# Kernel tuning notes

Measured on AMD Instinct MI355X. Metric: run time of the kernel, lower is better.

Reference implementation:

```python
import jax, jax.numpy as jnp
import numpy as np

B, CIN, NH, W, L, K = 16, 64, 64, 32, 4, 5
EPS = 1e-5
FORGET_BIAS = 1.0


def conv(x, w, b=None):
    # x: [B,C,H,W], w: [O,I,k,k] -> SAME padding, stride 1 (NCHW)
    y = jax.lax.conv_general_dilated(x, w, (1, 1), 'SAME',
                                     dimension_numbers=('NCHW', 'OIHW', 'NCHW'))
    if b is not None:
        y = y + b[None, :, None, None]
    return y


def ln(x, g, b):
    # torch LayerNorm([C,W,W]): normalize each sample over (C,H,W)
    m = jnp.mean(x, axis=(1, 2, 3), keepdims=True)
    v = jnp.mean((x - m) ** 2, axis=(1, 2, 3), keepdims=True)
    return (x - m) * jax.lax.rsqrt(v + EPS) * g[None] + b[None]


def attn_channel(q, kv):
    # q: [B,C,W,H], kv: [B,L,C,W,H]
    b, c, w, h = q.shape
    qf = q.reshape(b, c, w * h)                 # [B,C,HW]
    kf = kv.reshape(b, -1, w * h)               # [B,L*C,HW]
    a = jax.nn.softmax(jnp.einsum('bcp,blp->bcl', qf, kf), axis=2)  # [B,C,L*C]
    out = jnp.einsum('bcl,blp->bcp', a, kf)     # [B,C,HW]
    return out.reshape(b, c, w, h)


def attn_spatial(q, kv):
    # q: [B,C,W,H], kv: [B,L,C,W,H]
    b, c, w, h = q.shape
    qf = q.reshape(b, c, w * h).transpose(0, 2, 1)          # [B,HW,C]
    kf = kv.transpose(0, 1, 3, 4, 2).reshape(b, -1, c)      # [B,L*HW,C]
    a = jax.nn.softmax(jnp.einsum('bpc,bqc->bpq', qf, kf), axis=2)  # [B,HW,L*HW]
    out = jnp.einsum('bpq,bqc->bpc', a, kf)                 # [B,HW,C]
    return out.reshape(b, w, h, c).transpose(0, 3, 1, 2)


def setup_inputs() -> dict:
    key = jax.random.key(0)
    ks = iter(jax.random.split(key, 64))
    rn = lambda shape, s=1.0: jax.random.normal(next(ks), shape, jnp.float32) * s
    ones = lambda shape: jnp.ones(shape, jnp.float32)
    zeros = lambda shape: jnp.zeros(shape, jnp.float32)
    s = 0.02
    d = {}
    d['x_t'] = rn((B, CIN, W, W))
    d['h_t'] = rn((B, NH, W, W))
    d['c_t'] = rn((B, NH, W, W))
    d['c_historys'] = rn((B, L, NH, W, W))
    d['m_t'] = rn((B, NH, W, W))
    d['w_x'] = rn((7 * NH, CIN, K, K), s); d['ln_x_g'] = ones((7 * NH, W, W)); d['ln_x_b'] = zeros((7 * NH, W, W))
    d['w_h'] = rn((4 * NH, NH, K, K), s);  d['ln_h_g'] = ones((4 * NH, W, W)); d['ln_h_b'] = zeros((4 * NH, W, W))
    d['w_m'] = rn((3 * NH, NH, K, K), s);  d['ln_m_g'] = ones((3 * NH, W, W)); d['ln_m_b'] = zeros((3 * NH, W, W))
    d['w_o'] = rn((NH, 2 * NH, K, K), s);  d['ln_o_g'] = ones((NH, W, W));     d['ln_o_b'] = zeros((NH, W, W))
    d['w_last'] = rn((NH, 2 * NH, 1, 1), s)
    d['s_norm_g'] = ones((NH, W, W)); d['s_norm_b'] = zeros((NH, W, W))
    d['c_norm_g'] = ones((NH, W, W)); d['c_norm_b'] = zeros((NH, W, W))
    d['ca_w1'] = rn((NH, NH, K, K), s); d['ca_b1'] = zeros((NH,))
    d['ca_ln_g'] = ones((NH, W, W));    d['ca_ln_b'] = zeros((NH, W, W))
    d['ca_w2'] = rn((NH, NH, 1, 1), s); d['ca_b2'] = zeros((NH,))
    d['sa_w1'] = rn((NH, NH, K, K), s)
    d['sa_ln_g'] = ones((NH, W, W));    d['sa_ln_b'] = zeros((NH, W, W))
    d['sa_w2'] = rn((NH, NH, 1, 1), s)
    d['attn_w'] = rn((NH, NH, 1, 1), s)
    return d


def reference(x_t, h_t, c_t, c_historys, m_t,
              w_x, ln_x_g, ln_x_b, w_h, ln_h_g, ln_h_b, w_m, ln_m_g, ln_m_b,
              w_o, ln_o_g, ln_o_b, w_last,
              s_norm_g, s_norm_b, c_norm_g, c_norm_b,
              ca_w1, ca_b1, ca_ln_g, ca_ln_b, ca_w2, ca_b2,
              sa_w1, sa_ln_g, sa_ln_b, sa_w2, attn_w):
    x_concat = ln(conv(x_t, w_x), ln_x_g, ln_x_b)
    h_concat = ln(conv(h_t, w_h), ln_h_g, ln_h_b)
    m_concat = ln(conv(m_t, w_m), ln_m_g, ln_m_b)
    (i_x, f_x, g_x, i_xp, f_xp, g_xp, o_x) = jnp.split(x_concat, 7, axis=1)
    (i_h, f_h, g_h, o_h) = jnp.split(h_concat, 4, axis=1)
    (i_m, f_m, g_m) = jnp.split(m_concat, 3, axis=1)

    i_t = jax.nn.sigmoid(i_x + i_h)
    f_t = jax.nn.sigmoid(f_x + f_h + FORGET_BIAS)
    g_t = jnp.tanh(g_x + g_h)

    # attn_sum_fussion(c_t, query=f_t, keys=c_historys, values=c_historys)
    sp = ln(c_t + attn_spatial(f_t, c_historys), s_norm_g, s_norm_b)
    ch = ln(c_t + attn_channel(f_t, c_historys), c_norm_g, c_norm_b)
    s_a = conv(jax.nn.relu(ln(conv(sp, sa_w1), sa_ln_g, sa_ln_b)), sa_w2)
    c_a = conv(jax.nn.relu(ln(conv(ch, ca_w1, ca_b1), ca_ln_g, ca_ln_b)), ca_w2, ca_b2)
    attn = conv(s_a + c_a, attn_w)
    c_new = attn + i_t * g_t

    i_tp = jax.nn.sigmoid(i_xp + i_m)
    f_tp = jax.nn.sigmoid(f_xp + f_m + FORGET_BIAS)
    g_tp = jnp.tanh(g_xp + g_m)
    m_new = f_tp * m_t + i_tp * g_tp

    mem = jnp.concatenate((c_new, m_new), axis=1)
    o_t = jax.nn.sigmoid(o_x + o_h + ln(conv(mem, w_o), ln_o_g, ln_o_b))
    h_new = o_t * jnp.tanh(conv(mem, w_last))
    return h_new, c_new, m_new
```

## Files before the change

### kernel.cpp

```cpp
#include <hip/hip_runtime.h>
#include <hip/hip_bf16.h>

#define N1 (1u << 20)

typedef __attribute__((ext_vector_type(8))) short s8v;
typedef __attribute__((ext_vector_type(4))) float f4v;

static __device__ __forceinline__ float sigm(float x){ return 1.f/(1.f + __expf(-x)); }
static __device__ __forceinline__ float tanh_(float x){ return 1.f - 2.f/(__expf(2.f*x) + 1.f); }

static __device__ __forceinline__ ushort f2b(float f){
  union { float f; uint u; } x; x.f = f;
  uint r = x.u + 0x7FFFu + ((x.u >> 16) & 1u);
  return (ushort)(r >> 16);
}

static __device__ __forceinline__ void red_atomic2(float s, float q, float* d, int b, int t){
  #pragma unroll
  for (int m = 32; m; m >>= 1){ s += __shfl_xor(s, m); q += __shfl_xor(q, m); }
  if ((t & 63) == 0){ atomicAdd(&d[b*2], s); atomicAdd(&d[b*2+1], q); }
}

__global__ void k_zero(float* __restrict__ p){ p[threadIdx.x] = 0.f; }

__global__ __launch_bounds__(256) void k_wprep3(
    const float* __restrict__ sA, ushort* __restrict__ dA, int CoA, int CiA, int nA,
    const float* __restrict__ sB, ushort* __restrict__ dB, int CoB, int CiB, int nB,
    const float* __restrict__ sC, ushort* __restrict__ dC, int CoC, int CiC, int nC)
{
  int idx = blockIdx.x*256 + threadIdx.x;
  const float* s; ushort* d; int Co, Ci;
  if (idx < nA){ s=sA; d=dA; Co=CoA; Ci=CiA; }
  else if ((idx -= nA) < nB){ s=sB; d=dB; Co=CoB; Ci=CiB; }
  else if ((idx -= nB) < nC){ s=sC; d=dC; Co=CoC; Ci=CiC; }
  else return;
  int ci = idx % Ci; int r = idx / Ci; int co = r % Co; int tap = r / Co;
  d[idx] = f2b(s[((size_t)(co*Ci + ci))*25 + tap]);
}

struct Seg {
  const float* in; const ushort* w; const float* bias;
  float* out; float* ostat; const float* istat;
  const float* g; const float* bb;
  int Cin, Cout; float invN;
};
struct Segs3 { Seg s[3]; int b1, b2; };

template<int MT>
__global__ __launch_bounds__(256, 2) void k_convX(Segs3 Sg)
{
  constexpr int CO  = MT*16;
  constexpr int NW  = 5*CO*4;
  constexpr int ITW = (NW + 255) / 256;

  const int b = blockIdx.y;
  const int cog = blockIdx.x >> 2, pxblk = blockIdx.x & 3;
  const int si = (cog >= Sg.b1) + (cog >= Sg.b2);
  const Seg sg = Sg.s[si];
  const int base = si == 0 ? 0 : (si == 1 ? Sg.b1 : Sg.b2);
  const int co0 = (cog - base) * CO;
  const int r0 = pxblk << 3;
  const int t = threadIdx.x, w = t >> 6, l = t & 63;
  const int lane16 = l & 15, quad = l >> 4;

  __shared__ __align__(16) ushort S_[4][12][36][8];
  __shared__ __align__(16) ushort W_[2][4][5][CO][8];

  f4v acc[MT][4];
  #pragma unroll
  for (int mi = 0; mi < MT; ++mi)
    #pragma unroll
    for (int n = 0; n < 4; ++n) acc[mi][n] = (f4v){0.f,0.f,0.f,0.f};

  float mean = 0.f, rstd = 0.f;
  if (sg.istat){
    float s0 = sg.istat[b*2], s1 = sg.istat[b*2+1];
    mean = s0 * sg.invN;
    rstd = rsqrtf(s1 * sg.invN - mean*mean + 1e-5f);
  }

  const int ncc = sg.Cin >> 5;
  for (int cc = 0; cc < ncc; ++cc){
    __syncthreads();
    for (int idx = t; idx < 432; idx += 256){
      const int row = idx / 36, col = idx - row*36;
      const int ir = r0 - 2 + row, ic = col - 2;
      uint4 pk[4] = {make_uint4(0,0,0,0),make_uint4(0,0,0,0),make_uint4(0,0,0,0),make_uint4(0,0,0,0)};
      if ((unsigned)ir < 32u && (unsigned)ic < 32u){
        const int pix = (ir << 5) + ic;
        const float* bp = sg.in + (((size_t)(b*sg.Cin + (cc<<5))) << 10) + pix;
        #pragma unroll
        for (int q = 0; q < 4; ++q){
          uint hw[4];
          #pragma unroll
          for (int jj = 0; jj < 4; ++jj){
            const int c0 = q*8 + jj*2;
            float v0 = bp[(size_t)c0 << 10];
            float v1 = bp[(size_t)(c0+1) << 10];
            if (sg.g){
              const size_t li0 = (((size_t)((cc<<5)+c0)) << 10) + pix;
              v0 = (v0 - mean)*rstd*sg.g[li0] + sg.bb[li0];
              v1 = (v1 - mean)*rstd*sg.g[li0+1024] + sg.bb[li0+1024];
            }
            hw[jj] = (uint)f2b(v0) | ((uint)f2b(v1) << 16);
          }
          pk[q] = make_uint4(hw[0], hw[1], hw[2], hw[3]);
        }
      }
      #pragma unroll
      for (int q = 0; q < 4; ++q) *(uint4*)&S_[q][row][col][0] = pk[q];
    }
    #pragma unroll
    for (int it = 0; it < ITW; ++it){
      const int idx = t + it*256;
      if (ITW*256 == NW || idx < NW){
        const int q = idx & 3, r = idx >> 2;
        const int co = r & (CO - 1), dx = r / CO;
        uint4 wv = *(const uint4*)(sg.w + ((size_t)(dx*sg.Cout + co0+co))*sg.Cin + (cc<<5) + (q<<3));
        *(uint4*)&W_[0][q][dx][co][0] = wv;
      }
    }
    __syncthreads();
    for (int dy = 0; dy < 5; ++dy){
      uint4 wreg[ITW];
      if (dy < 4){
        #pragma unroll
        for (int it = 0; it < ITW; ++it){
          const int idx = t + it*256;
          if (ITW*256 == NW || idx < NW){
            const int q = idx & 3, r = idx >> 2;
            const int co = r & (CO - 1), dx = r / CO;
            wreg[it] = *(const uint4*)(sg.w + ((size_t)(((dy+1)*5+dx)*sg.Cout + co0+co))*sg.Cin + (cc<<5) + (q<<3));
          }
        }
      }
      #pragma unroll
      for (int dx = 0; dx < 5; ++dx){
        s8v a[MT];
        #pragma unroll
        for (int mi = 0; mi < MT; ++mi)
          a[mi] = *(const s8v*)&W_[dy & 1][quad][dx][mi*16 + lane16][0];
        #pragma unroll
        for (int n = 0; n < 4; ++n){
          const int srow = (w<<1) + (n>>1) + dy;
          const int col = ((n&1)<<4) + lane16 + dx;
          s8v bb = *(const s8v*)&S_[quad][srow][col][0];
          #pragma unroll
          for (int mi = 0; mi < MT; ++mi)
            acc[mi][n] = __builtin_amdgcn_mfma_f32_16x16x32_bf16(a[mi], bb, acc[mi][n], 0, 0, 0);
        }
      }
      if (dy < 4){
        #pragma unroll
        for (int it = 0; it < ITW; ++it){
          const int idx = t + it*256;
          if (ITW*256 == NW || idx < NW){
            const int q = idx & 3, r = idx >> 2;
            const int co = r & (CO - 1), dx = r / CO;
            *(uint4*)&W_[(dy+1) & 1][q][dx][co][0] = wreg[it];
          }
        }
      }
      __syncthreads();
    }
  }
  float lsum = 0.f, lsq = 0.f;
  #pragma unroll
  for (int mi = 0; mi < MT; ++mi){
    const int co = co0 + mi*16 + (quad<<2);
    #pragma unroll
    for (int n = 0; n < 4; ++n){
      const int row = r0 + (w<<1) + (n>>1);
      const int col = ((n&1)<<4) + lane16;
      #pragma unroll
      for (int i = 0; i < 4; ++i){
        float v = acc[mi][n][i] + (sg.bias ? sg.bias[co+i] : 0.f);
        sg.out[(((size_t)(b*sg.Cout + co + i)) << 10) + (row<<5) + col] = v;
        lsum += v; lsq += v*v;
      }
    }
  }
  if (sg.ostat) red_atomic2(lsum, lsq, sg.ostat, b, t);
}

__global__ __launch_bounds__(256) void k_prep(const float* __restrict__ src,
                                              ushort* __restrict__ outC,
                                              ushort* __restrict__ outT)
{
  const int plane = blockIdx.y;
  const int p0 = blockIdx.x << 6;
  const float* sp = src + ((size_t)plane << 16);
  __shared__ __align__(16) float T[64][68];
  const int t = threadIdx.x, c = t >> 2, g = t & 3;
  #pragma unroll
  for (int i = 0; i < 4; ++i){
    float4 f = *(const float4*)(sp + ((size_t)c << 10) + p0 + (g << 4) + (i << 2));
    *(float4*)&T[c][(g << 4) + (i << 2)] = f;
    if (outC){
      uint2 pk2;
      pk2.x = (uint)f2b(f.x) | ((uint)f2b(f.y) << 16);
      pk2.y = (uint)f2b(f.z) | ((uint)f2b(f.w) << 16);
      *(uint2*)(outC + ((((size_t)plane << 6) + c) << 10) + p0 + (g << 4) + (i << 2)) = pk2;
    }
  }
  __syncthreads();
  const int p = t >> 2, c0 = (t & 3) << 4;
  uint w4[8];
  #pragma unroll
  for (int k = 0; k < 8; ++k){
    ushort lo = f2b(T[c0 + 2*k][p]);
    ushort hi = f2b(T[c0 + 2*k + 1][p]);
    w4[k] = (uint)lo | ((uint)hi << 16);
  }
  ushort* dst = outT + ((((size_t)plane << 10) + p0 + p) << 6) + c0;
  *(uint4*)(dst)     = *(uint4*)&w4[0];
  *(uint4*)(dst + 8) = *(uint4*)&w4[4];
}

__global__ __launch_bounds__(256) void k_gates(
    const float* __restrict__ bufx, const float* __restrict__ bufh, const float* __restrict__ bufm,
    const float* __restrict__ lnxg, const float* __restrict__ lnxb,
    const float* __restrict__ lnhg, const float* __restrict__ lnhb,
    const float* __restrict__ lnmg, const float* __restrict__ lnmb,
    const float* __restrict__ m_t, const float* __restrict__ stats,
    float* __restrict__ ft, float* __restrict__ ig, float* __restrict__ osum,
    float* __restrict__ memo, float* __restrict__ out_m)
{
  const int idx = blockIdx.x*256 + threadIdx.x;
  const int b = idx >> 16, rem = idx & 65535;
  const int c = rem >> 10, p = rem & 1023;

  float mx = stats[b*2]      * (1.f/458752.f);
  float vx = stats[b*2+1]    * (1.f/458752.f) - mx*mx;  float rx = rsqrtf(vx + 1e-5f);
  float mh = stats[32+b*2]   * (1.f/262144.f);
  float vh = stats[32+b*2+1] * (1.f/262144.f) - mh*mh;  float rh = rsqrtf(vh + 1e-5f);
  float mm = stats[64+b*2]   * (1.f/196608.f);
  float vm = stats[64+b*2+1] * (1.f/196608.f) - mm*mm;  float rm = rsqrtf(vm + 1e-5f);

  auto LX = [&](int k){
    size_t ch = (size_t)k*64 + c; size_t gi = ((size_t)b*448 + ch)*1024 + p; size_t li = ch*1024 + p;
    return (bufx[gi] - mx)*rx*lnxg[li] + lnxb[li]; };
  auto LH = [&](int k){
    size_t ch = (size_t)k*64 + c; size_t gi = ((size_t)b*256 + ch)*1024 + p; size_t li = ch*1024 + p;
    return (bufh[gi] - mh)*rh*lnhg[li] + lnhb[li]; };
  auto LM = [&](int k){
    size_t ch = (size_t)k*64 + c; size_t gi = ((size_t)b*192 + ch)*1024 + p; size_t li = ch*1024 + p;
    return (bufm[gi] - mm)*rm*lnmg[li] + lnmb[li]; };

  float i_t = sigm(LX(0) + LH(0));
  float f_t = sigm(LX(1) + LH(1) + 1.f);
  float g_t = tanh_(LX(2) + LH(2));
  float i_p = sigm(LX(3) + LM(0));
  float f_p = sigm(LX(4) + LM(1) + 1.f);
  float g_p = tanh_(LX(5) + LM(2));
  float ox = LX(6), oh = LH(3);

  ft[idx]   = f_t;
  ig[idx]   = i_t * g_t;
  osum[idx] = ox + oh;
  float mn = f_p * m_t[idx] + i_p * g_p;
  out_m[idx] = mn;
  memo[((size_t)(b*128 + 64 + c) << 10) + p] = mn;
}

__global__ __launch_bounds__(256) void k_spat_mfma(
    const ushort* __restrict__ qT, const ushort* __restrict__ kvC, const ushort* __restrict__ kvT,
    const float* __restrict__ c_t, float* __restrict__ sp_raw, float* __restrict__ stats)
{
  const int p0 = blockIdx.x << 6, b = blockIdx.y;
  const int t = threadIdx.x, w = t >> 6, l = t & 63;
  const int lane16 = l & 15, quad = l >> 4;
  __shared__ __align__(16) ushort Kt[64][72];
  __shared__ __align__(16) ushort Kc[64][72];
  __shared__ __align__(16) ushort Eb[64][72];
  __shared__ __align__(16) float  XO[64][65];

  s8v qa0, qa1;
  {
    const ushort* qr = qT + ((((size_t)b << 10) + p0 + (w << 4) + lane16) << 6) + (quad << 3);
    qa0 = *(const s8v*)(qr);
    qa1 = *(const s8v*)(qr + 32);
  }
  f4v o0 = {0.f,0.f,0.f,0.f}, o1 = o0, o2 = o0, o3 = o0, dacc = o0;
  const short oneb = (short)0x3F80;
  const s8v ones = { oneb, oneb, oneb, oneb, oneb, oneb, oneb, oneb };

  const int r = t >> 2, g4 = (t & 3) << 4;
  for (int chunk = 0; chunk < 64; ++chunk){
    const int lidx = chunk >> 4, pk = (chunk & 15) << 6;
    __syncthreads();
    {
      const ushort* sc = kvC + ((((size_t)(b*4 + lidx) << 6) + r) << 10) + pk + g4;
      *(uint4*)&Kc[r][g4]     = *(const uint4*)(sc);
      *(uint4*)&Kc[r][g4 + 8] = *(const uint4*)(sc + 8);
      const ushort* st = kvT + ((((size_t)(b*4 + lidx) << 10) + pk + r) << 6) + g4;
      *(uint4*)&Kt[r][g4]     = *(const uint4*)(st);
      *(uint4*)&Kt[r][g4 + 8] = *(const uint4*)(st + 8);
    }
    __syncthreads();
    #pragma unroll
    for (int nt = 0; nt < 4; ++nt){
      const ushort* bt = &Kt[(nt << 4) + lane16][quad << 3];
      s8v b0 = *(const s8v*)(bt);
      s8v b1 = *(const s8v*)(bt + 32);
      f4v s = {0.f,0.f,0.f,0.f};
      s = __builtin_amdgcn_mfma_f32_16x16x32_bf16(qa0, b0, s, 0, 0, 0);
      s = __builtin_amdgcn_mfma_f32_16x16x32_bf16(qa1, b1, s, 0, 0, 0);
      #pragma unroll
      for (int i = 0; i < 4; ++i){
        float e = __expf(s[i] - 12.f);
        Eb[(w << 4) + (quad << 2) + i][(nt << 4) + lane16] = f2b(e);
      }
    }
    __syncthreads();
    #pragma unroll
    for (int ks = 0; ks < 2; ++ks){
      s8v ea = *(const s8v*)&Eb[(w << 4) + lane16][(ks << 5) + (quad << 3)];
      dacc = __builtin_amdgcn_mfma_f32_16x16x32_bf16(ea, ones, dacc, 0, 0, 0);
      s8v bc0 = *(const s8v*)&Kc[ 0 + lane16][(ks << 5) + (quad << 3)];
      s8v bc1 = *(const s8v*)&Kc[16 + lane16][(ks << 5) + (quad << 3)];
      s8v bc2 = *(const s8v*)&Kc[32 + lane16][(ks << 5) + (quad << 3)];
      s8v bc3 = *(const s8v*)&Kc[48 + lane16][(ks << 5) + (quad << 3)];
      o0 = __builtin_amdgcn_mfma_f32_16x16x32_bf16(ea, bc0, o0, 0, 0, 0);
      o1 = __builtin_amdgcn_mfma_f32_16x16x32_bf16(ea, bc1, o1, 0, 0, 0);
      o2 = __builtin_amdgcn_mfma_f32_16x16x32_bf16(ea, bc2, o2, 0, 0, 0);
      o3 = __builtin_amdgcn_mfma_f32_16x16x32_bf16(ea, bc3, o3, 0, 0, 0);
    }
  }
  {
    float inv0 = 1.f/dacc[0], inv1 = 1.f/dacc[1], inv2 = 1.f/dacc[2], inv3 = 1.f/dacc[3];
    const int pxl = (w << 4) + (quad << 2);
    XO[ 0 + lane16][pxl+0] = o0[0]*inv0; XO[ 0 + lane16][pxl+1] = o0[1]*inv1;
    XO[ 0 + lane16][pxl+2] = o0[2]*inv2; XO[ 0 + lane16][pxl+3] = o0[3]*inv3;
    XO[16 + lane16][pxl+0] = o1[0]*inv0; XO[16 + lane16][pxl+1] = o1[1]*inv1;
    XO[16 + lane16][pxl+2] = o1[2]*inv2; XO[16 + lane16][pxl+3] = o1[3]*inv3;
    XO[32 + lane16][pxl+0] = o2[0]*inv0; XO[32 + lane16][pxl+1] = o2[1]*inv1;
    XO[32 + lane16][pxl+2] = o2[2]*inv2; XO[32 + lane16][pxl+3] = o2[3]*inv3;
    XO[48 + lane16][pxl+0] = o3[0]*inv0; XO[48 + lane16][pxl+1] = o3[1]*inv1;
    XO[48 + lane16][pxl+2] = o3[2]*inv2; XO[48 + lane16][pxl+3] = o3[3]*inv3;
  }
  __syncthreads();
  {
    const int ch = t >> 2;
    float lsum = 0.f, lsq = 0.f;
    #pragma unroll
    for (int i = 0; i < 4; ++i){
      size_t gi = ((size_t)b << 16) + ((size_t)ch << 10) + p0 + g4 + (i << 2);
      float4 cv = *(const float4*)(c_t + gi);
      float4 ov;
      ov.x = cv.x + XO[ch][g4 + (i << 2) + 0];
      ov.y = cv.y + XO[ch][g4 + (i << 2) + 1];
      ov.z = cv.z + XO[ch][g4 + (i << 2) + 2];
      ov.w = cv.w + XO[ch][g4 + (i << 2) + 3];
      *(float4*)(sp_raw + gi) = ov;
      lsum += ov.x + ov.y + ov.z + ov.w;
      lsq  += ov.x*ov.x + ov.y*ov.y + ov.z*ov.z + ov.w*ov.w;
    }
    red_atomic2(lsum, lsq, stats, b, t);
  }
}

__global__ __launch_bounds__(256) void k_chlog_m(
    const ushort* __restrict__ ftC, const ushort* __restrict__ kvC, float* __restrict__ lg)
{
  const int lp = blockIdx.x, b = blockIdx.y;
  const int t = threadIdx.x, w = t >> 6, l = t & 63;
  const int lane16 = l & 15, quad = l >> 4;
  __shared__ __align__(16) ushort As[8][64][8];
  __shared__ __align__(16) ushort Bs[8][128][8];
  f4v acc[4][2];
  #pragma unroll
  for (int mi = 0; mi < 4; ++mi){ acc[mi][0] = (f4v){0.f,0.f,0.f,0.f}; acc[mi][1] = (f4v){0.f,0.f,0.f,0.f}; }

  for (int kc = 0; kc < 16; ++kc){
    __syncthreads();
    #pragma unroll
    for (int it = 0; it < 2; ++it){
      const int idx = t + it*256;
      const int c = idx >> 3, q = idx & 7;
      *(uint4*)&As[q][c][0] = *(const uint4*)(ftC + (((size_t)(b*64 + c)) << 10) + (kc<<6) + (q<<3));
    }
    #pragma unroll
    for (int it = 0; it < 4; ++it){
      const int idx = t + it*256;
      const int r2 = idx >> 3, q = idx & 7;
      const int plane = (b<<2) + (lp<<1) + (r2>>6);
      *(uint4*)&Bs[q][r2][0] = *(const uint4*)(kvC + ((((size_t)plane << 6) + (r2 & 63)) << 10) + (kc<<6) + (q<<3));
    }
    __syncthreads();
    #pragma unroll
    for (int ks = 0; ks < 2; ++ks){
      s8v a[4];
      #pragma unroll
      for (int mi = 0; mi < 4; ++mi)
        a[mi] = *(const s8v*)&As[(ks<<2)+quad][mi*16 + lane16][0];
      #pragma unroll
      for (int nt = 0; nt < 2; ++nt){
        s8v bb = *(const s8v*)&Bs[(ks<<2)+quad][(w<<5) + (nt<<4) + lane16][0];
        #pragma unroll
        for (int mi = 0; mi < 4; ++mi)
          acc[mi][nt] = __builtin_amdgcn_mfma_f32_16x16x32_bf16(a[mi], bb, acc[mi][nt], 0, 0, 0);
      }
    }
  }
  #pragma unroll
  for (int mi = 0; mi < 4; ++mi)
    #pragma unroll
    for (int nt = 0; nt < 2; ++nt)
      #pragma unroll
      for (int i = 0; i < 4; ++i){
        const int c = mi*16 + (quad<<2) + i;
        const int n = (lp<<7) + (w<<5) + (nt<<4) + lane16;
        lg[(((size_t)(b*64 + c)) << 8) + n] = acc[mi][nt][i];
      }
}

__global__ __launch_bounds__(256) void k_chsm(const float* __restrict__ a, ushort* __restrict__ ab)
{
  const int row  = blockIdx.x*4 + (threadIdx.x >> 6);
  const int lane = threadIdx.x & 63;
  const float* rp = a + ((size_t)row << 8);
  float v0 = rp[lane], v1 = rp[lane+64], v2 = rp[lane+128], v3 = rp[lane+192];
  float mx = fmaxf(fmaxf(v0, v1), fmaxf(v2, v3));
  #pragma unroll
  for (int m = 32; m; m >>= 1) mx = fmaxf(mx, __shfl_xor(mx, m));
  v0 = __expf(v0 - mx); v1 = __expf(v1 - mx); v2 = __expf(v2 - mx); v3 = __expf(v3 - mx);
  float s = v0 + v1 + v2 + v3;
  #pragma unroll
  for (int m = 32; m; m >>= 1) s += __shfl_xor(s, m);
  float inv = 1.f / s;
  ushort* op = ab + ((size_t)row << 8);
  op[lane] = f2b(v0*inv); op[lane+64] = f2b(v1*inv);
  op[lane+128] = f2b(v2*inv); op[lane+192] = f2b(v3*inv);
}

__global__ __launch_bounds__(256) void k_chout_m(
    const ushort* __restrict__ chlb, const ushort* __restrict__ kvT,
    const float* __restrict__ c_t, float* __restrict__ ch_raw, float* __restrict__ stats)
{
  const int p0 = blockIdx.x << 7, b = blockIdx.y;
  const int t = threadIdx.x, w = t >> 6, l = t & 63;
  const int lane16 = l & 15, quad = l >> 4;
  __shared__ __align__(16) ushort As[32][64][8];
  __shared__ __align__(16) ushort Bs[32][32][8];
  #pragma unroll
  for (int it = 0; it < 8; ++it){
    const int idx = t + it*256;
    const int c = idx >> 5, q = idx & 31;
    *(uint4*)&As[q][c][0] = *(const uint4*)(chlb + (((size_t)(b*64 + c)) << 8) + (q<<3));
  }
  __syncthreads();
  s8v a[8];
  #pragma unroll
  for (int ks = 0; ks < 8; ++ks)
    a[ks] = *(const s8v*)&As[(ks<<2)+quad][(w<<4) + lane16][0];
  float lsum = 0.f, lsq = 0.f;
  for (int pc = 0; pc < 4; ++pc){
    __syncthreads();
    #pragma unroll
    for (int it = 0; it < 4; ++it){
      const int idx = t + it*256;
      const int px = idx >> 5, q = idx & 31;
      const int plane = (b<<2) + (q>>3);
      *(uint4*)&Bs[q][px][0] = *(const uint4*)(kvT + ((((size_t)plane << 10) + p0 + (pc<<5) + px) << 6) + ((q&7)<<3));
    }
    __syncthreads();
    #pragma unroll
    for (int nt = 0; nt < 2; ++nt){
      f4v o = {0.f,0.f,0.f,0.f};
      #pragma unroll
      for (int ks = 0; ks < 8; ++ks){
        s8v bb = *(const s8v*)&Bs[(ks<<2)+quad][(nt<<4) + lane16][0];
        o = __builtin_amdgcn_mfma_f32_16x16x32_bf16(a[ks], bb, o, 0, 0, 0);
      }
      #pragma unroll
      for (int i = 0; i < 4; ++i){
        const int c = (w<<4) + (quad<<2) + i;
        const int px = p0 + (pc<<5) + (nt<<4) + lane16;
        size_t gi = ((size_t)b << 16) + ((size_t)c << 10) + px;
        float v = c_t[gi] + o[i];
        ch_raw[gi] = v;
        lsum += v; lsq += v*v;
      }
    }
  }
  red_atomic2(lsum, lsq, stats, b, t);
}

__global__ __launch_bounds__(256) void k_attnfinal(
    const float* __restrict__ samid, const float* __restrict__ camid,
    const float* __restrict__ stats_sa, const float* __restrict__ stats_ca,
    const float* __restrict__ salng, const float* __restrict__ salnb,
    const float* __restrict__ calng, const float* __restrict__ calnb,
    const float* __restrict__ wsa2, const float* __restrict__ wca2,
    const float* __restrict__ cab2, const float* __restrict__ wat,
    const float* __restrict__ ig, float* __restrict__ out_c, float* __restrict__ memo)
{
  const int p0 = blockIdx.x << 6, b = blockIdx.y, t = threadIdx.x;
  const int tc = t & 15, tp = t >> 4;
  __shared__ __align__(16) float R[64][68];
  __shared__ __align__(16) float Wl[64][68];
  __shared__ __align__(16) float Ms[64][68];
  const float invN = 1.f/65536.f;
  float acc[4][4] = {};
  #pragma unroll
  for (int pass = 0; pass < 2; ++pass){
    const float* mid = pass ? camid : samid;
    const float* st  = pass ? stats_ca : stats_sa;
    const float* g   = pass ? calng : salng;
    const float* bb  = pass ? calnb : salnb;
    const float* w   = pass ? wca2  : wsa2;
    float mean = st[b*2]*invN;
    float var  = st[b*2+1]*invN - mean*mean;
    float rstd = rsqrtf(var + 1e-5f);
    __syncthreads();
    {
      const int j = t & 63, c0 = t >> 6;
      for (int ci = c0; ci < 64; ci += 4){
        size_t gi = ((size_t)b << 16) + ((size_t)ci << 10) + p0 + j;
        size_t li = ((size_t)ci << 10) + p0 + j;
        float v = (mid[gi] - mean)*rstd*g[li] + bb[li];
        R[ci][j] = fmaxf(v, 0.f);
      }
      const int ci2 = t & 63, c20 = t >> 6;
      for (int c2 = c20; c2 < 64; c2 += 4) Wl[ci2][c2] = w[((size_t)c2 << 6) + ci2];
    }
    __syncthreads();
    for (int ci = 0; ci < 64; ++ci){
      float wv[4], rv[4];
      *(float4*)wv = *(const float4*)&Wl[ci][4*tc];
      *(float4*)rv = *(const float4*)&R[ci][4*tp];
      #pragma unroll
      for (int i = 0; i < 4; ++i)
        #pragma unroll
        for (int j = 0; j < 4; ++j)
          acc[i][j] = fmaf(wv[i], rv[j], acc[i][j]);
    }
  }
  {
    float b2[4];
    #pragma unroll
    for (int i = 0; i < 4; ++i) b2[i] = cab2[4*tc + i];
    #pragma unroll
    for (int i = 0; i < 4; ++i)
      #pragma unroll
      for (int j = 0; j < 4; ++j)
        Ms[4*tc+i][4*tp+j] = acc[i][j] + b2[i];
  }
  __syncthreads();
  {
    const int ci2 = t & 63, c20 = t >> 6;
    for (int c2 = c20; c2 < 64; c2 += 4) Wl[ci2][c2] = wat[((size_t)c2 << 6) + ci2];
  }
  __syncthreads();
  float acc2[4][4] = {};
  for (int c2 = 0; c2 < 64; ++c2){
    float wv[4], mv[4];
    *(float4*)wv = *(const float4*)&Wl[c2][4*tc];
    *(float4*)mv = *(const float4*)&Ms[c2][4*tp];
    #pragma unroll
    for (int i = 0; i < 4; ++i)
      #pragma unroll
      for (int j = 0; j < 4; ++j)
        acc2[i][j] = fmaf(wv[i], mv[j], acc2[i][j]);
  }
  #pragma unroll
  for (int i = 0; i < 4; ++i)
    #pragma unroll
    for (int j = 0; j < 4; ++j){
      size_t gi = ((size_t)b << 16) + ((size_t)(4*tc + i) << 10) + p0 + 4*tp + j;
      float v = acc2[i][j] + ig[gi];
      out_c[gi] = v;
      memo[((size_t)(b*128 + 4*tc + i) << 10) + p0 + 4*tp + j] = v;
    }
}

__global__ __launch_bounds__(256) void k_final(
    const float* __restrict__ memo, const float* __restrict__ wlast,
    const float* __restrict__ bufo, const float* __restrict__ osum,
    const float* __restrict__ stats_o, const float* __restrict__ lnog, const float* __restrict__ lnob,
    float* __restrict__ out_h)
{
  const int p0 = blockIdx.x << 6, b = blockIdx.y, t = threadIdx.x;
  const int tc = t & 15, tp = t >> 4;
  __shared__ __align__(16) float Msh[64][68];
  __shared__ __align__(16) float Wt[64][68];
  float acc[4][4] = {};
  #pragma unroll
  for (int half = 0; half < 2; ++half){
    __syncthreads();
    {
      const int j = t & 63, c0 = t >> 6;
      for (int ci = c0; ci < 64; ci += 4)
        Msh[ci][j] = memo[((size_t)(b*128 + half*64 + ci) << 10) + p0 + j];
      const int ci2 = t & 63, co0 = t >> 6;
      for (int co = co0; co < 64; co += 4) Wt[ci2][co] = wlast[((size_t)co << 7) + half*64 + ci2];
    }
    __syncthreads();
    for (int ci = 0; ci < 64; ++ci){
      float wv[4], mv[4];
      *(float4*)wv = *(const float4*)&Wt[ci][4*tc];
      *(float4*)mv = *(const float4*)&Msh[ci][4*tp];
      #pragma unroll
      for (int i = 0; i < 4; ++i)
        #pragma unroll
        for (int j = 0; j < 4; ++j)
          acc[i][j] = fmaf(wv[i], mv[j], acc[i][j]);
    }
  }
  float mean = stats_o[b*2]*(1.f/65536.f);
  float var  = stats_o[b*2+1]*(1.f/65536.f) - mean*mean;
  float rstd = rsqrtf(var + 1e-5f);
  #pragma unroll
  for (int i = 0; i < 4; ++i)
    #pragma unroll
    for (int j = 0; j < 4; ++j){
      const int co = 4*tc + i, p = p0 + 4*tp + j;
      size_t gi = ((size_t)b << 16) + ((size_t)co << 10) + p;
      size_t li = ((size_t)co << 10) + p;
      float lno = (bufo[gi] - mean)*rstd*lnog[li] + lnob[li];
      float o = sigm(osum[gi] + lno);
      out_h[gi] = o * tanh_(acc[i][j]);
    }
}

extern "C" void kernel_launch(void* const* d_in, const int* in_sizes, int n_in,
                              void* d_out, int out_size, void* d_ws, size_t ws_size,
                              hipStream_t stream)
{
  const float* x_t   = (const float*)d_in[0];
  const float* h_t   = (const float*)d_in[1];
  const float* c_t   = (const float*)d_in[2];
  const float* chist = (const float*)d_in[3];
  const float* m_t   = (const float*)d_in[4];
  const float* w_x   = (const float*)d_in[5];
  const float* lnxg  = (const float*)d_in[6];
  const float* lnxb  = (const float*)d_in[7];
  const float* w_h   = (const float*)d_in[8];
  const float* lnhg  = (const float*)d_in[9];
  const float* lnhb  = (const float*)d_in[10];
  const float* w_m   = (const float*)d_in[11];
  const float* lnmg  = (const float*)d_in[12];
  const float* lnmb  = (const float*)d_in[13];
  const float* w_o   = (const float*)d_in[14];
  const float* lnog  = (const float*)d_in[15];
  const float* lnob  = (const float*)d_in[16];
  const float* w_last= (const float*)d_in[17];
  const float* sng   = (const float*)d_in[18];
  const float* snb   = (const float*)d_in[19];
  const float* cng   = (const float*)d_in[20];
  const float* cnb   = (const float*)d_in[21];
  const float* ca_w1 = (const float*)d_in[22];
  const float* ca_b1 = (const float*)d_in[23];
  const float* calng = (const float*)d_in[24];
  const float* calnb = (const float*)d_in[25];
  const float* ca_w2 = (const float*)d_in[26];
  const float* ca_b2 = (const float*)d_in[27];
  const float* sa_w1 = (const float*)d_in[28];
  const float* salng = (const float*)d_in[29];
  const float* salnb = (const float*)d_in[30];
  const float* sa_w2 = (const float*)d_in[31];
  const float* attn_w= (const float*)d_in[32];

  float* out = (float*)d_out;
  float* ws  = (float*)d_ws;

  float* stats = ws;
  float* bufx  = ws + 1024;
  float* bufh  = bufx + 7*(size_t)N1;
  float* bufm  = bufh + 4*(size_t)N1;
  float* ft    = bufm + 3*(size_t)N1;
  float* ig    = ft   + (size_t)N1;
  float* osum  = ig   + (size_t)N1;
  float* memo  = osum + (size_t)N1;
  float* sp    = bufx;
  float* ch    = bufx + (size_t)N1;
  float* samid = bufx + 2*(size_t)N1;
  float* camid = bufx + 3*(size_t)N1;
  float* bufo  = bufx + 4*(size_t)N1;
  float* chl   = bufx + 5*(size_t)N1;
  ushort* kvC  = (ushort*)bufh;
  ushort* kvT  = kvC + 4*(size_t)N1;
  ushort* qT   = (ushort*)bufm;
  ushort* ftC  = qT + (size_t)N1;

  ushort* wbx = (ushort*)ft;
  ushort* wbh = wbx + 716800;
  ushort* wbm = wbh + 409600;
  ushort* wbo  = (ushort*)(chl + 262144);
  ushort* wbsa = wbo + 204800;
  ushort* wbca = wbsa + 102400;
  ushort* chlb = wbca + 102400;

  float* out_h = out;
  float* out_c = out + (size_t)N1;
  float* out_m = out + 2*(size_t)N1;

  k_zero<<<dim3(1), dim3(256), 0, stream>>>(stats);

  k_wprep3<<<dim3(5600), dim3(256), 0, stream>>>(
      w_x, wbx, 448, 64, 716800,
      w_h, wbh, 256, 64, 409600,
      w_m, wbm, 192, 64, 307200);

  {
    Segs3 XHM;
    XHM.s[0] = Seg{ x_t, wbx, nullptr, bufx, stats+0,  nullptr, nullptr, nullptr, 64, 448, 0.f };
    XHM.s[1] = Seg{ h_t, wbh, nullptr, bufh, stats+32, nullptr, nullptr, nullptr, 64, 256, 0.f };
    XHM.s[2] = Seg{ m_t, wbm, nullptr, bufm, stats+64, nullptr, nullptr, nullptr, 64, 192, 0.f };
    XHM.b1 = 7; XHM.b2 = 11;
    k_convX<4><<<dim3(56,16), dim3(256), 0, stream>>>(XHM);
  }

  k_gates<<<dim3(4096), dim3(256), 0, stream>>>(bufx, bufh, bufm, lnxg, lnxb, lnhg, lnhb,
                                                lnmg, lnmb, m_t, stats,
                                                ft, ig, osum, memo, out_m);

  k_wprep3<<<dim3(1600), dim3(256), 0, stream>>>(
      w_o,   wbo,  64, 128, 204800,
      sa_w1, wbsa, 64,  64, 102400,
      ca_w1, wbca, 64,  64, 102400);

  k_prep<<<dim3(16,64), dim3(256), 0, stream>>>(chist, kvC, kvT);
  k_prep<<<dim3(16,16), dim3(256), 0, stream>>>(ft, ftC, qT);

  k_spat_mfma<<<dim3(16,16), dim3(256), 0, stream>>>(qT, kvC, kvT, c_t, sp, stats+96);
  k_chlog_m<<<dim3(2,16), dim3(256), 0, stream>>>(ftC, kvC, chl);
  k_chsm  <<<dim3(256),  dim3(256), 0, stream>>>(chl, chlb);
  k_chout_m<<<dim3(8,16), dim3(256), 0, stream>>>(chlb, kvT, c_t, ch, stats+128);

  {
    Segs3 SC;
    SC.s[0] = Seg{ sp, wbsa, nullptr, samid, stats+160, stats+96,  sng, snb, 64, 64, 1.f/65536.f };
    SC.s[1] = Seg{ ch, wbca, ca_b1,   camid, stats+192, stats+128, cng, cnb, 64, 64, 1.f/65536.f };
    SC.s[2] = SC.s[1];
    SC.b1 = 2; SC.b2 = 1000;
    k_convX<2><<<dim3(16,16), dim3(256), 0, stream>>>(SC);
  }

  k_attnfinal<<<dim3(16,16), dim3(256), 0, stream>>>(samid, camid, stats+160, stats+192,
                                                     salng, salnb, calng, calnb,
                                                     sa_w2, ca_w2, ca_b2, attn_w,
                                                     ig, out_c, memo);

  {
    Segs3 O;
    O.s[0] = Seg{ memo, wbo, nullptr, bufo, stats+224, nullptr, nullptr, nullptr, 128, 64, 0.f };
    O.s[1] = O.s[0]; O.s[2] = O.s[0];
    O.b1 = 1000; O.b2 = 1000;
    k_convX<2><<<dim3(8,16), dim3(256), 0, stream>>>(O);
  }

  k_final<<<dim3(16,16), dim3(256), 0, stream>>>(memo, w_last, bufo, osum, stats+224,
                                                 lnog, lnob, out_h);
}
```

Before: 526.0 us.

## Load conv weights directly into registers, vectorize gates, widen conv tiles

The convolution kernel stops staging weights through double-buffered shared memory. Each lane now loads its MFMA A-operand weights straight from global memory (or cache) per dy row, which removes the per-dy __syncthreads and the LDS write traffic. The gates kernel now handles four pixels per thread with float4 loads and stores, so it launches a quarter as many blocks. The smaller convs move to MT=4, which halves their block counts. The trade-off is more global or L2 weight loads, redundant across waves and pixel blocks, higher register pressure from holding 5×MT weight vectors, and lower occupancy for the small convs.

```diff
diff --git a/kernel.cpp b/kernel.cpp
--- a/kernel.cpp
+++ b/kernel.cpp
@@ -47,24 +47,19 @@
 struct Segs3 { Seg s[3]; int b1, b2; };
 
 template<int MT>
-__global__ __launch_bounds__(256, 2) void k_convX(Segs3 Sg)
-{
-  constexpr int CO  = MT*16;
-  constexpr int NW  = 5*CO*4;
-  constexpr int ITW = (NW + 255) / 256;
-
+__global__ __launch_bounds__(256, 2) void k_convW(Segs3 Sg)
+{
   const int b = blockIdx.y;
   const int cog = blockIdx.x >> 2, pxblk = blockIdx.x & 3;
   const int si = (cog >= Sg.b1) + (cog >= Sg.b2);
   const Seg sg = Sg.s[si];
   const int base = si == 0 ? 0 : (si == 1 ? Sg.b1 : Sg.b2);
-  const int co0 = (cog - base) * CO;
+  const int co0 = (cog - base) * (MT*16);
   const int r0 = pxblk << 3;
   const int t = threadIdx.x, w = t >> 6, l = t & 63;
   const int lane16 = l & 15, quad = l >> 4;
 
   __shared__ __align__(16) ushort S_[4][12][36][8];
-  __shared__ __align__(16) ushort W_[2][4][5][CO][8];
 
   f4v acc[MT][4];
   #pragma unroll
@@ -78,6 +73,10 @@
     mean = s0 * sg.invN;
     rstd = rsqrtf(s1 * sg.invN - mean*mean + 1e-5f);
   }
+
+  const ushort* wlane = sg.w + (size_t)(co0 + lane16)*sg.Cin + (quad<<3);
+  const size_t co_step = (size_t)16*sg.Cin;
+  const size_t tap_step = (size_t)sg.Cout*sg.Cin;
 
   const int ncc = sg.Cin >> 5;
   for (int cc = 0; cc < ncc; ++cc){
@@ -110,36 +109,17 @@
       #pragma unroll
       for (int q = 0; q < 4; ++q) *(uint4*)&S_[q][row][col][0] = pk[q];
     }
-    #pragma unroll
-    for (int it = 0; it < ITW; ++it){
-      const int idx = t + it*256;
-      if (ITW*256 == NW || idx < NW){
-        const int q = idx & 3, r = idx >> 2;
-        const int co = r & (CO - 1), dx = r / CO;
-        uint4 wv = *(const uint4*)(sg.w + ((size_t)(dx*sg.Cout + co0+co))*sg.Cin + (cc<<5) + (q<<3));
-        *(uint4*)&W_[0][q][dx][co][0] = wv;
-      }
-    }
-    __syncthreads();
+    __syncthreads();
+    const ushort* wcc = wlane + ((size_t)cc << 5);
     for (int dy = 0; dy < 5; ++dy){
-      uint4 wreg[ITW];
-      if (dy < 4){
-        #pragma unroll
-        for (int it = 0; it < ITW; ++it){
-          const int idx = t + it*256;
-          if (ITW*256 == NW || idx < NW){
-            const int q = idx & 3, r = idx >> 2;
-            const int co = r & (CO - 1), dx = r / CO;
-            wreg[it] = *(const uint4*)(sg.w + ((size_t)(((dy+1)*5+dx)*sg.Cout + co0+co))*sg.Cin + (cc<<5) + (q<<3));
-          }
-        }
-      }
-      #pragma unroll
-      for (int dx = 0; dx < 5; ++dx){
-        s8v a[MT];
+      s8v a[5][MT];
+      #pragma unroll
+      for (int dx = 0; dx < 5; ++dx)
         #pragma unroll
         for (int mi = 0; mi < MT; ++mi)
-          a[mi] = *(const s8v*)&W_[dy & 1][quad][dx][mi*16 + lane16][0];
+          a[dx][mi] = *(const s8v*)(wcc + (size_t)(dy*5+dx)*tap_step + (size_t)mi*co_step);
+      #pragma unroll
+      for (int dx = 0; dx < 5; ++dx){
         #pragma unroll
         for (int n = 0; n < 4; ++n){
           const int srow = (w<<1) + (n>>1) + dy;
@@ -147,21 +127,9 @@
           s8v bb = *(const s8v*)&S_[quad][srow][col][0];
           #pragma unroll
           for (int mi = 0; mi < MT; ++mi)
-            acc[mi][n] = __builtin_amdgcn_mfma_f32_16x16x32_bf16(a[mi], bb, acc[mi][n], 0, 0, 0);
+            acc[mi][n] = __builtin_amdgcn_mfma_f32_16x16x32_bf16(a[dx][mi], bb, acc[mi][n], 0, 0, 0);
         }
       }
-      if (dy < 4){
-        #pragma unroll
-        for (int it = 0; it < ITW; ++it){
-          const int idx = t + it*256;
-          if (ITW*256 == NW || idx < NW){
-            const int q = idx & 3, r = idx >> 2;
-            const int co = r & (CO - 1), dx = r / CO;
-            *(uint4*)&W_[(dy+1) & 1][q][dx][co][0] = wreg[it];
-          }
-        }
-      }
-      __syncthreads();
     }
   }
   float lsum = 0.f, lsq = 0.f;
@@ -227,8 +195,8 @@
     float* __restrict__ memo, float* __restrict__ out_m)
 {
   const int idx = blockIdx.x*256 + threadIdx.x;
-  const int b = idx >> 16, rem = idx & 65535;
-  const int c = rem >> 10, p = rem & 1023;
+  const int b = idx >> 14, rem = idx & 16383;
+  const int c = rem >> 8, p = (rem & 255) << 2;
 
   float mx = stats[b*2]      * (1.f/458752.f);
   float vx = stats[b*2+1]    * (1.f/458752.f) - mx*mx;  float rx = rsqrtf(vx + 1e-5f);
@@ -237,30 +205,61 @@
   float mm = stats[64+b*2]   * (1.f/196608.f);
   float vm = stats[64+b*2+1] * (1.f/196608.f) - mm*mm;  float rm = rsqrtf(vm + 1e-5f);
 
+  auto LN4 = [&](const float* x, const float* g, const float* bb, size_t gi, size_t li,
+                 float mean, float rstd){
+    float4 v = *(const float4*)(x+gi);
+    float4 gg = *(const float4*)(g+li);
+    float4 b4 = *(const float4*)(bb+li);
+    float4 r;
+    r.x = (v.x-mean)*rstd*gg.x + b4.x;
+    r.y = (v.y-mean)*rstd*gg.y + b4.y;
+    r.z = (v.z-mean)*rstd*gg.z + b4.z;
+    r.w = (v.w-mean)*rstd*gg.w + b4.w;
+    return r;
+  };
   auto LX = [&](int k){
-    size_t ch = (size_t)k*64 + c; size_t gi = ((size_t)b*448 + ch)*1024 + p; size_t li = ch*1024 + p;
-    return (bufx[gi] - mx)*rx*lnxg[li] + lnxb[li]; };
+    size_t ch = (size_t)k*64 + c;
+    return LN4(bufx, lnxg, lnxb, ((size_t)b*448 + ch)*1024 + p, ch*1024 + p, mx, rx); };
   auto LH = [&](int k){
-    size_t ch = (size_t)k*64 + c; size_t gi = ((size_t)b*256 + ch)*1024 + p; size_t li = ch*1024 + p;
-    return (bufh[gi] - mh)*rh*lnhg[li] + lnhb[li]; };
+    size_t ch = (size_t)k*64 + c;
+    return LN4(bufh, lnhg, lnhb, ((size_t)b*256 + ch)*1024 + p, ch*1024 + p, mh, rh); };
   auto LM = [&](int k){
-    size_t ch = (size_t)k*64 + c; size_t gi = ((size_t)b*192 + ch)*1024 + p; size_t li = ch*1024 + p;
-    return (bufm[gi] - mm)*rm*lnmg[li] + lnmb[li]; };
-
-  float i_t = sigm(LX(0) + LH(0));
-  float f_t = sigm(LX(1) + LH(1) + 1.f);
-  float g_t = tanh_(LX(2) + LH(2));
-  float i_p = sigm(LX(3) + LM(0));
-  float f_p = sigm(LX(4) + LM(1) + 1.f);
-  float g_p = tanh_(LX(5) + LM(2));
-  float ox = LX(6), oh = LH(3);
-
-  ft[idx]   = f_t;
-  ig[idx]   = i_t * g_t;
-  osum[idx] = ox + oh;
-  float mn = f_p * m_t[idx] + i_p * g_p;
-  out_m[idx] = mn;
-  memo[((size_t)(b*128 + 64 + c) << 10) + p] = mn;
+    size_t ch = (size_t)k*64 + c;
+    return LN4(bufm, lnmg, lnmb, ((size_t)b*192 + ch)*1024 + p, ch*1024 + p, mm, rm); };
+
+  float4 ixv=LX(0), fxv=LX(1), gxv=LX(2), ipv=LX(3), fpv=LX(4), gpv=LX(5), oxv=LX(6);
+  float4 ihv=LH(0), fhv=LH(1), ghv=LH(2), ohv=LH(3);
+  float4 imv=LM(0), fmv=LM(1), gmv=LM(2);
+  const size_t gbase = ((size_t)b << 16) + ((size_t)c << 10) + p;
+  float4 mt4 = *(const float4*)(m_t + gbase);
+
+  float4 ftv, igv, osv, mnv;
+  {
+    float* fo = &ftv.x; float* io = &igv.x; float* oo = &osv.x; float* mo = &mnv.x;
+    const float* pix = &ixv.x; const float* pfx = &fxv.x; const float* pgx = &gxv.x;
+    const float* pip = &ipv.x; const float* pfp = &fpv.x; const float* pgp = &gpv.x;
+    const float* pox = &oxv.x; const float* pih = &ihv.x; const float* pfh = &fhv.x;
+    const float* pgh = &ghv.x; const float* poh = &ohv.x; const float* pim = &imv.x;
+    const float* pfm = &fmv.x; const float* pgm = &gmv.x; const float* pmt = &mt4.x;
+    #pragma unroll
+    for (int j = 0; j < 4; ++j){
+      float i_t = sigm(pix[j] + pih[j]);
+      float f_t = sigm(pfx[j] + pfh[j] + 1.f);
+      float g_t = tanh_(pgx[j] + pgh[j]);
+      float i_p = sigm(pip[j] + pim[j]);
+      float f_p = sigm(pfp[j] + pfm[j] + 1.f);
+      float g_p = tanh_(pgp[j] + pgm[j]);
+      fo[j] = f_t;
+      io[j] = i_t * g_t;
+      oo[j] = pox[j] + poh[j];
+      mo[j] = f_p * pmt[j] + i_p * g_p;
+    }
+  }
+  *(float4*)(ft + gbase)   = ftv;
+  *(float4*)(ig + gbase)   = igv;
+  *(float4*)(osum + gbase) = osv;
+  *(float4*)(out_m + gbase)= mnv;
+  *(float4*)(memo + ((size_t)(b*128 + 64 + c) << 10) + p) = mnv;
 }
 
 __global__ __launch_bounds__(256) void k_spat_mfma(
@@ -709,10 +708,10 @@
     XHM.s[1] = Seg{ h_t, wbh, nullptr, bufh, stats+32, nullptr, nullptr, nullptr, 64, 256, 0.f };
     XHM.s[2] = Seg{ m_t, wbm, nullptr, bufm, stats+64, nullptr, nullptr, nullptr, 64, 192, 0.f };
     XHM.b1 = 7; XHM.b2 = 11;
-    k_convX<4><<<dim3(56,16), dim3(256), 0, stream>>>(XHM);
-  }
-
-  k_gates<<<dim3(4096), dim3(256), 0, stream>>>(bufx, bufh, bufm, lnxg, lnxb, lnhg, lnhb,
+    k_convW<4><<<dim3(56,16), dim3(256), 0, stream>>>(XHM);
+  }
+
+  k_gates<<<dim3(1024), dim3(256), 0, stream>>>(bufx, bufh, bufm, lnxg, lnxb, lnhg, lnhb,
                                                 lnmg, lnmb, m_t, stats,
                                                 ft, ig, osum, memo, out_m);
 
@@ -734,8 +733,8 @@
     SC.s[0] = Seg{ sp, wbsa, nullptr, samid, stats+160, stats+96,  sng, snb, 64, 64, 1.f/65536.f };
     SC.s[1] = Seg{ ch, wbca, ca_b1,   camid, stats+192, stats+128, cng, cnb, 64, 64, 1.f/65536.f };
     SC.s[2] = SC.s[1];
-    SC.b1 = 2; SC.b2 = 1000;
-    k_convX<2><<<dim3(16,16), dim3(256), 0, stream>>>(SC);
+    SC.b1 = 1; SC.b2 = 1000;
+    k_convW<4><<<dim3(8,16), dim3(256), 0, stream>>>(SC);
   }
 
   k_attnfinal<<<dim3(16,16), dim3(256), 0, stream>>>(samid, camid, stats+160, stats+192,
@@ -748,7 +747,7 @@
     O.s[0] = Seg{ memo, wbo, nullptr, bufo, stats+224, nullptr, nullptr, nullptr, 128, 64, 0.f };
     O.s[1] = O.s[0]; O.s[2] = O.s[0];
     O.b1 = 1000; O.b2 = 1000;
-    k_convX<2><<<dim3(8,16), dim3(256), 0, stream>>>(O);
+    k_convW<4><<<dim3(4,16), dim3(256), 0, stream>>>(O);
   }
 
   k_final<<<dim3(16,16), dim3(256), 0, stream>>>(memo, w_last, bufo, osum, stats+224,
```

Result: slower. 612.0 us (+16.3%).
